# Optimization experiments

Hardware: AMD Instinct MI355X
Metric: run time of the kernel (lower is better)

Reference implementation:

```python
import jax, jax.numpy as jnp
import numpy as np

EMB_DIM = 256
NUM_HEADS = 4
HEAD_DIM = EMB_DIM // NUM_HEADS
N_EDGES = 320000
N_NODES = 10000
EPS = 1e-16  # torch_geometric softmax epsilon


def setup_inputs() -> dict:
    key = jax.random.key(0)
    kq, kk, ki, kw1, kb1, kw2 = jax.random.split(key, 6)
    q = jax.random.normal(kq, (N_EDGES, EMB_DIM), dtype=jnp.float32)
    k = jax.random.normal(kk, (N_EDGES, EMB_DIM), dtype=jnp.float32)
    index = jnp.sort(jax.random.randint(ki, (N_EDGES,), 0, N_NODES, dtype=jnp.int32))
    # xavier_uniform with gain 1/sqrt(2)
    lim1 = (1.0 / np.sqrt(2.0)) * np.sqrt(6.0 / (2 * EMB_DIM + EMB_DIM))
    w1_w = jax.random.uniform(kw1, (EMB_DIM, 2 * EMB_DIM), dtype=jnp.float32, minval=-lim1, maxval=lim1)
    w1_b = jnp.zeros((EMB_DIM,), dtype=jnp.float32)
    lim2 = (1.0 / np.sqrt(2.0)) * np.sqrt(6.0 / (NUM_HEADS + HEAD_DIM))
    w2 = jax.random.uniform(kw2, (NUM_HEADS, HEAD_DIM), dtype=jnp.float32, minval=-lim2, maxval=lim2)
    return {"q": q, "k": k, "w1_w": w1_w, "w1_b": w1_b, "w2": w2,
            "index": index, "dim_size": N_NODES}


def _segment_softmax(src, index, num_segments):
    # src: [E, H, 1]; index: [E] segment ids; stable softmax per segment per head
    seg_max = jax.ops.segment_max(src, index, num_segments=num_segments)  # [N, H, 1]
    out = jnp.exp(src - seg_max[index])
    seg_sum = jax.ops.segment_sum(out, index, num_segments=num_segments)  # [N, H, 1]
    return out / (seg_sum[index] + EPS)


def reference(q, k, w1_w, w1_b, w2, index, dim_size):
    x = jnp.concatenate([q, k], axis=1)                      # [E, 2D]
    x = x @ w1_w.T + w1_b                                    # [E, D]
    x = jax.nn.leaky_relu(x, negative_slope=0.01)
    x = x.reshape(-1, NUM_HEADS, HEAD_DIM)                   # [E, H, C]
    attn = jnp.einsum('nhc,hc->nh', x, w2)[..., None]        # [E, H, 1]
    return _segment_softmax(attn, index, dim_size)
```

## Files before the change

kernel.cpp:

```cpp
#include <hip/hip_runtime.h>
#include <hip/hip_bf16.h>


typedef __attribute__((ext_vector_type(8))) short bf16x8;
typedef __attribute__((ext_vector_type(4))) float f32x4;
typedef __attribute__((ext_vector_type(4))) short s16x4;

#define NNODES 10000

__device__ __forceinline__ short f2bf(float f) {
    __hip_bfloat16 h = __float2bfloat16(f);
    return *reinterpret_cast<short*>(&h);
}

__device__ __forceinline__ void gload_lds16(const void* g, void* l) {
    __builtin_amdgcn_global_load_lds(
        (const __attribute__((address_space(1))) unsigned int*)g,
        (__attribute__((address_space(3))) unsigned int*)l, 16, 0, 0);
}

__global__ void w1_cvt(const float* __restrict__ w1, short* __restrict__ w1b) {
    int i = (blockIdx.x * 256 + threadIdx.x) * 4;
    float4 v = *(const float4*)(w1 + i);
    s16x4 o; o[0] = f2bf(v.x); o[1] = f2bf(v.y); o[2] = f2bf(v.z); o[3] = f2bf(v.w);
    *(s16x4*)(w1b + i) = o;
}

__global__ __launch_bounds__(512, 4) void attn_gemm(
    const float* __restrict__ q, const float* __restrict__ kk_,
    const short* __restrict__ w1b, const float* __restrict__ b1,
    const float* __restrict__ w2, float* __restrict__ attn)
{
    __shared__ float lds_a[2][4096];
    __shared__ short lds_b[2][8192];

    const int tid  = threadIdx.x;
    const int lane = tid & 63;
    const int w    = tid >> 6;
    const int wm   = w >> 1;
    const int wn   = w & 1;
    const int l15  = lane & 15;
    const int lhi  = lane >> 4;
    const int row0 = blockIdx.x * 128;

    const int a_row  = w * 8 + (lane >> 3);
    const int a_csrc = (lane & 7) ^ (lane >> 3);
    const int b_d    = w * 16 + (lane >> 2);
    const int b_csrc = (lane & 3) ^ ((lane >> 3) & 3);

    f32x4 acc[2][8];
#pragma unroll
    for (int i = 0; i < 2; ++i)
#pragma unroll
        for (int j = 0; j < 8; ++j) acc[i][j] = (f32x4){0.f, 0.f, 0.f, 0.f};

    size_t a_off[2], b_off[2];
#pragma unroll
    for (int i = 0; i < 2; ++i) {
        a_off[i] = (size_t)(row0 + i * 64 + a_row) * 256 + a_csrc * 4;
        b_off[i] = (size_t)(i * 128 + b_d) * 512 + b_csrc * 8;
    }

#define STAGE(buf, kt)                                                          \
    {                                                                           \
        const float* abase = ((kt) < 8) ? q : kk_;                              \
        const int koff = ((kt) & 7) * 32;                                       \
        gload_lds16(abase + a_off[0] + koff,                                    \
                    (char*)&lds_a[buf][0] + (0 * 8 + w) * 1024);                \
        gload_lds16(abase + a_off[1] + koff,                                    \
                    (char*)&lds_a[buf][0] + (1 * 8 + w) * 1024);                \
        gload_lds16(w1b + b_off[0] + (kt) * 32,                                 \
                    (char*)&lds_b[buf][0] + (0 * 8 + w) * 1024);                \
        gload_lds16(w1b + b_off[1] + (kt) * 32,                                 \
                    (char*)&lds_b[buf][0] + (1 * 8 + w) * 1024);                \
    }

    STAGE(0, 0);
    __syncthreads();

#pragma unroll
    for (int kt = 0; kt < 16; ++kt) {
        const int cur = kt & 1;
        if (kt < 15) STAGE(cur ^ 1, kt + 1);

        bf16x8 af[2];
#pragma unroll
        for (int fm = 0; fm < 2; ++fm) {
            const int r = wm * 32 + fm * 16 + l15;
            const float* As = &lds_a[cur][r * 32];
            f32x4 a0 = *(const f32x4*)(As + (((2 * lhi)     ^ (r & 7)) * 4));
            f32x4 a1 = *(const f32x4*)(As + (((2 * lhi + 1) ^ (r & 7)) * 4));
            bf16x8 pk;
            pk[0] = f2bf(a0[0]); pk[1] = f2bf(a0[1]); pk[2] = f2bf(a0[2]); pk[3] = f2bf(a0[3]);
            pk[4] = f2bf(a1[0]); pk[5] = f2bf(a1[1]); pk[6] = f2bf(a1[2]); pk[7] = f2bf(a1[3]);
            af[fm] = pk;
        }
#pragma unroll
        for (int fn = 0; fn < 8; ++fn) {
            const int d = wn * 128 + fn * 16 + l15;
            bf16x8 bfv = *(const bf16x8*)(&lds_b[cur][d * 32 + ((lhi ^ ((d >> 1) & 3)) * 8)]);
            acc[0][fn] = __builtin_amdgcn_mfma_f32_16x16x32_bf16(af[0], bfv, acc[0][fn], 0, 0, 0);
            acc[1][fn] = __builtin_amdgcn_mfma_f32_16x16x32_bf16(af[1], bfv, acc[1][fn], 0, 0, 0);
        }
        __syncthreads();
    }
#undef STAGE

    float bias[8], w2v[8];
#pragma unroll
    for (int fn = 0; fn < 8; ++fn) {
        int col = wn * 128 + fn * 16 + l15;
        bias[fn] = b1[col];
        w2v[fn]  = w2[col];
    }
#pragma unroll
    for (int fm = 0; fm < 2; ++fm) {
#pragma unroll
        for (int r = 0; r < 4; ++r) {
            int row = row0 + wm * 32 + fm * 16 + lhi * 4 + r;
            float p0 = 0.f, p1 = 0.f;
#pragma unroll
            for (int fn = 0; fn < 4; ++fn) {
                float y = acc[fm][fn][r] + bias[fn];
                y = (y > 0.f) ? y : 0.01f * y;
                p0 += y * w2v[fn];
            }
#pragma unroll
            for (int fn = 4; fn < 8; ++fn) {
                float y = acc[fm][fn][r] + bias[fn];
                y = (y > 0.f) ? y : 0.01f * y;
                p1 += y * w2v[fn];
            }
#pragma unroll
            for (int m = 1; m < 16; m <<= 1) {
                p0 += __shfl_xor(p0, m);
                p1 += __shfl_xor(p1, m);
            }
            if (l15 == 0) {
                attn[(size_t)row * 4 + wn * 2 + 0] = p0;
                attn[(size_t)row * 4 + wn * 2 + 1] = p1;
            }
        }
    }
}

__device__ __forceinline__ unsigned fenc(float f) {
    unsigned u = __float_as_uint(f);
    return (u & 0x80000000u) ? ~u : (u | 0x80000000u);
}
__device__ __forceinline__ float fdec(unsigned k) {
    return (k & 0x80000000u) ? __uint_as_float(k ^ 0x80000000u) : __uint_as_float(~k);
}

__global__ void seg_init(unsigned* __restrict__ segmax, float* __restrict__ segsum, int n) {
    int i = blockIdx.x * blockDim.x + threadIdx.x;
    if (i < n) { segmax[i] = 0u; segsum[i] = 0.f; }
}

__global__ void seg_max(const float* __restrict__ attn, const int* __restrict__ index,
                        unsigned* __restrict__ segmax, int total) {
    int i = blockIdx.x * blockDim.x + threadIdx.x;
    if (i >= total) return;
    int e = i >> 2, h = i & 3;
    atomicMax(&segmax[index[e] * 4 + h], fenc(attn[i]));
}

__global__ void seg_expsum(float* __restrict__ attn, const int* __restrict__ index,
                           const unsigned* __restrict__ segmax, float* __restrict__ segsum,
                           int total) {
    int i = blockIdx.x * blockDim.x + threadIdx.x;
    if (i >= total) return;
    int e = i >> 2, h = i & 3;
    float m = fdec(segmax[index[e] * 4 + h]);
    float ex = expf(attn[i] - m);
    attn[i] = ex;
    atomicAdd(&segsum[index[e] * 4 + h], ex);
}

__global__ void seg_norm(const float* __restrict__ attn, const int* __restrict__ index,
                         const float* __restrict__ segsum, float* __restrict__ out, int total) {
    int i = blockIdx.x * blockDim.x + threadIdx.x;
    if (i >= total) return;
    int e = i >> 2, h = i & 3;
    out[i] = attn[i] / (segsum[index[e] * 4 + h] + 1e-16f);
}

extern "C" void kernel_launch(void* const* d_in, const int* in_sizes, int n_in,
                              void* d_out, int out_size, void* d_ws, size_t ws_size,
                              hipStream_t stream) {
    const float* q   = (const float*)d_in[0];
    const float* k   = (const float*)d_in[1];
    const float* w1  = (const float*)d_in[2];
    const float* b1  = (const float*)d_in[3];
    const float* w2  = (const float*)d_in[4];
    const int* index = (const int*)d_in[5];

    const int nE = in_sizes[0] / 256;
    char* ws = (char*)d_ws;
    float*    attn   = (float*)ws;                       ws += (size_t)nE * 4 * 4;
    unsigned* segmax = (unsigned*)ws;                    ws += (size_t)NNODES * 4 * 4;
    float*    segsum = (float*)ws;                       ws += (size_t)NNODES * 4 * 4;
    short*    w1bf   = (short*)ws;
    float*    out    = (float*)d_out;

    w1_cvt<<<128, 256, 0, stream>>>(w1, w1bf);

    int nseg = NNODES * 4;
    seg_init<<<(nseg + 255) / 256, 256, 0, stream>>>(segmax, segsum, nseg);

    attn_gemm<<<nE / 128, 512, 0, stream>>>(q, k, w1bf, b1, w2, attn);

    int total = nE * 4;
    int blks = (total + 255) / 256;
    seg_max<<<blks, 256, 0, stream>>>(attn, index, segmax, total);
    seg_expsum<<<blks, 256, 0, stream>>>(attn, index, segmax, segsum, total);
    seg_norm<<<blks, 256, 0, stream>>>(attn, index, segsum, out, total);
}
```

Before: 220.1 us.

## Fuse exp and segment-sum into GEMM epilogue, drop segment-max pass

Removes the segment max reduction and computes exp(logit) directly in the GEMM epilogue, atomically accumulating per-segment sums there, leaving only a normalization kernel. The A operand is now loaded through registers, converted to bf16 before staging into LDS, and the wave tiling is changed so each wave covers one head. This eliminates two elementwise passes and their atomics, but drops the max subtraction, so large logits could overflow exp.

```diff
diff --git a/kernel.cpp b/kernel.cpp
--- a/kernel.cpp
+++ b/kernel.cpp
@@ -26,155 +26,128 @@
     *(s16x4*)(w1b + i) = o;
 }
 
+__global__ void seg_init(float* __restrict__ segsum, int n) {
+    int i = blockIdx.x * blockDim.x + threadIdx.x;
+    if (i < n) segsum[i] = 0.f;
+}
+
 __global__ __launch_bounds__(512, 4) void attn_gemm(
     const float* __restrict__ q, const float* __restrict__ kk_,
     const short* __restrict__ w1b, const float* __restrict__ b1,
-    const float* __restrict__ w2, float* __restrict__ attn)
+    const float* __restrict__ w2, const int* __restrict__ index,
+    float* __restrict__ attn, float* __restrict__ segsum)
 {
-    __shared__ float lds_a[2][4096];
-    __shared__ short lds_b[2][8192];
+    __shared__ short lds_a[2][128 * 32];
+    __shared__ short lds_b[2][256 * 32];
 
     const int tid  = threadIdx.x;
     const int lane = tid & 63;
     const int w    = tid >> 6;
-    const int wm   = w >> 1;
-    const int wn   = w & 1;
+    const int wm   = w >> 2;
+    const int wn   = w & 3;
     const int l15  = lane & 15;
     const int lhi  = lane >> 4;
     const int row0 = blockIdx.x * 128;
 
-    const int a_row  = w * 8 + (lane >> 3);
-    const int a_csrc = (lane & 7) ^ (lane >> 3);
     const int b_d    = w * 16 + (lane >> 2);
     const int b_csrc = (lane & 3) ^ ((lane >> 3) & 3);
+    const size_t b_off0 = (size_t)b_d * 512 + b_csrc * 8;
+    const size_t b_off1 = (size_t)(128 + b_d) * 512 + b_csrc * 8;
+    const int b_dst0 = w * 1024 + lane * 16;
+    const int b_dst1 = (8 + w) * 1024 + lane * 16;
 
-    f32x4 acc[2][8];
+    const int a_r = tid >> 2;
+    const int a_c = tid & 3;
+    const size_t a_goff = (size_t)(row0 + a_r) * 256 + a_c * 8;
+    const int a_ldst = a_r * 32 + ((a_c ^ ((a_r >> 1) & 3)) * 8);
+
+    f32x4 acc[4][4];
 #pragma unroll
-    for (int i = 0; i < 2; ++i)
+    for (int i = 0; i < 4; ++i)
 #pragma unroll
-        for (int j = 0; j < 8; ++j) acc[i][j] = (f32x4){0.f, 0.f, 0.f, 0.f};
+        for (int j = 0; j < 4; ++j) acc[i][j] = (f32x4){0.f, 0.f, 0.f, 0.f};
 
-    size_t a_off[2], b_off[2];
-#pragma unroll
-    for (int i = 0; i < 2; ++i) {
-        a_off[i] = (size_t)(row0 + i * 64 + a_row) * 256 + a_csrc * 4;
-        b_off[i] = (size_t)(i * 128 + b_d) * 512 + b_csrc * 8;
+    {
+        gload_lds16(w1b + b_off0, (char*)&lds_b[0][0] + b_dst0);
+        gload_lds16(w1b + b_off1, (char*)&lds_b[0][0] + b_dst1);
+        float4 f0 = *(const float4*)(q + a_goff);
+        float4 f1 = *(const float4*)(q + a_goff + 4);
+        bf16x8 pk;
+        pk[0] = f2bf(f0.x); pk[1] = f2bf(f0.y); pk[2] = f2bf(f0.z); pk[3] = f2bf(f0.w);
+        pk[4] = f2bf(f1.x); pk[5] = f2bf(f1.y); pk[6] = f2bf(f1.z); pk[7] = f2bf(f1.w);
+        *(bf16x8*)&lds_a[0][a_ldst] = pk;
     }
-
-#define STAGE(buf, kt)                                                          \
-    {                                                                           \
-        const float* abase = ((kt) < 8) ? q : kk_;                              \
-        const int koff = ((kt) & 7) * 32;                                       \
-        gload_lds16(abase + a_off[0] + koff,                                    \
-                    (char*)&lds_a[buf][0] + (0 * 8 + w) * 1024);                \
-        gload_lds16(abase + a_off[1] + koff,                                    \
-                    (char*)&lds_a[buf][0] + (1 * 8 + w) * 1024);                \
-        gload_lds16(w1b + b_off[0] + (kt) * 32,                                 \
-                    (char*)&lds_b[buf][0] + (0 * 8 + w) * 1024);                \
-        gload_lds16(w1b + b_off[1] + (kt) * 32,                                 \
-                    (char*)&lds_b[buf][0] + (1 * 8 + w) * 1024);                \
-    }
-
-    STAGE(0, 0);
     __syncthreads();
 
 #pragma unroll
     for (int kt = 0; kt < 16; ++kt) {
-        const int cur = kt & 1;
-        if (kt < 15) STAGE(cur ^ 1, kt + 1);
+        const int cur = kt & 1, nxt = cur ^ 1;
 
-        bf16x8 af[2];
+        float4 f0, f1;
+        if (kt < 15) {
+            const float* abase = (kt + 1 < 8) ? q : kk_;
+            const int koff = ((kt + 1) & 7) * 32;
+            f0 = *(const float4*)(abase + a_goff + koff);
+            f1 = *(const float4*)(abase + a_goff + koff + 4);
+            gload_lds16(w1b + b_off0 + (size_t)(kt + 1) * 32, (char*)&lds_b[nxt][0] + b_dst0);
+            gload_lds16(w1b + b_off1 + (size_t)(kt + 1) * 32, (char*)&lds_b[nxt][0] + b_dst1);
+        }
+
+        bf16x8 af[4], bfv[4];
 #pragma unroll
-        for (int fm = 0; fm < 2; ++fm) {
-            const int r = wm * 32 + fm * 16 + l15;
-            const float* As = &lds_a[cur][r * 32];
-            f32x4 a0 = *(const f32x4*)(As + (((2 * lhi)     ^ (r & 7)) * 4));
-            f32x4 a1 = *(const f32x4*)(As + (((2 * lhi + 1) ^ (r & 7)) * 4));
-            bf16x8 pk;
-            pk[0] = f2bf(a0[0]); pk[1] = f2bf(a0[1]); pk[2] = f2bf(a0[2]); pk[3] = f2bf(a0[3]);
-            pk[4] = f2bf(a1[0]); pk[5] = f2bf(a1[1]); pk[6] = f2bf(a1[2]); pk[7] = f2bf(a1[3]);
-            af[fm] = pk;
+        for (int fm = 0; fm < 4; ++fm) {
+            const int r = wm * 64 + fm * 16 + l15;
+            af[fm] = *(const bf16x8*)&lds_a[cur][r * 32 + ((lhi ^ ((r >> 1) & 3)) * 8)];
         }
 #pragma unroll
-        for (int fn = 0; fn < 8; ++fn) {
-            const int d = wn * 128 + fn * 16 + l15;
-            bf16x8 bfv = *(const bf16x8*)(&lds_b[cur][d * 32 + ((lhi ^ ((d >> 1) & 3)) * 8)]);
-            acc[0][fn] = __builtin_amdgcn_mfma_f32_16x16x32_bf16(af[0], bfv, acc[0][fn], 0, 0, 0);
-            acc[1][fn] = __builtin_amdgcn_mfma_f32_16x16x32_bf16(af[1], bfv, acc[1][fn], 0, 0, 0);
+        for (int fn = 0; fn < 4; ++fn) {
+            const int d = wn * 64 + fn * 16 + l15;
+            bfv[fn] = *(const bf16x8*)&lds_b[cur][d * 32 + ((lhi ^ ((d >> 1) & 3)) * 8)];
+        }
+#pragma unroll
+        for (int fm = 0; fm < 4; ++fm)
+#pragma unroll
+            for (int fn = 0; fn < 4; ++fn)
+                acc[fm][fn] = __builtin_amdgcn_mfma_f32_16x16x32_bf16(
+                    af[fm], bfv[fn], acc[fm][fn], 0, 0, 0);
+
+        if (kt < 15) {
+            bf16x8 pk;
+            pk[0] = f2bf(f0.x); pk[1] = f2bf(f0.y); pk[2] = f2bf(f0.z); pk[3] = f2bf(f0.w);
+            pk[4] = f2bf(f1.x); pk[5] = f2bf(f1.y); pk[6] = f2bf(f1.z); pk[7] = f2bf(f1.w);
+            *(bf16x8*)&lds_a[nxt][a_ldst] = pk;
         }
         __syncthreads();
     }
-#undef STAGE
 
-    float bias[8], w2v[8];
+    float bias[4], w2v[4];
 #pragma unroll
-    for (int fn = 0; fn < 8; ++fn) {
-        int col = wn * 128 + fn * 16 + l15;
+    for (int fn = 0; fn < 4; ++fn) {
+        int col = wn * 64 + fn * 16 + l15;
         bias[fn] = b1[col];
         w2v[fn]  = w2[col];
     }
 #pragma unroll
-    for (int fm = 0; fm < 2; ++fm) {
+    for (int fm = 0; fm < 4; ++fm) {
 #pragma unroll
         for (int r = 0; r < 4; ++r) {
-            int row = row0 + wm * 32 + fm * 16 + lhi * 4 + r;
-            float p0 = 0.f, p1 = 0.f;
+            int row = row0 + wm * 64 + fm * 16 + lhi * 4 + r;
+            float p = 0.f;
 #pragma unroll
             for (int fn = 0; fn < 4; ++fn) {
                 float y = acc[fm][fn][r] + bias[fn];
                 y = (y > 0.f) ? y : 0.01f * y;
-                p0 += y * w2v[fn];
+                p += y * w2v[fn];
             }
 #pragma unroll
-            for (int fn = 4; fn < 8; ++fn) {
-                float y = acc[fm][fn][r] + bias[fn];
-                y = (y > 0.f) ? y : 0.01f * y;
-                p1 += y * w2v[fn];
-            }
-#pragma unroll
-            for (int m = 1; m < 16; m <<= 1) {
-                p0 += __shfl_xor(p0, m);
-                p1 += __shfl_xor(p1, m);
-            }
+            for (int m = 1; m < 16; m <<= 1) p += __shfl_xor(p, m);
             if (l15 == 0) {
-                attn[(size_t)row * 4 + wn * 2 + 0] = p0;
-                attn[(size_t)row * 4 + wn * 2 + 1] = p1;
+                float e = __expf(p);
+                attn[(size_t)row * 4 + wn] = e;
+                atomicAdd(&segsum[index[row] * 4 + wn], e);
             }
         }
     }
-}
-
-__device__ __forceinline__ unsigned fenc(float f) {
-    unsigned u = __float_as_uint(f);
-    return (u & 0x80000000u) ? ~u : (u | 0x80000000u);
-}
-__device__ __forceinline__ float fdec(unsigned k) {
-    return (k & 0x80000000u) ? __uint_as_float(k ^ 0x80000000u) : __uint_as_float(~k);
-}
-
-__global__ void seg_init(unsigned* __restrict__ segmax, float* __restrict__ segsum, int n) {
-    int i = blockIdx.x * blockDim.x + threadIdx.x;
-    if (i < n) { segmax[i] = 0u; segsum[i] = 0.f; }
-}
-
-__global__ void seg_max(const float* __restrict__ attn, const int* __restrict__ index,
-                        unsigned* __restrict__ segmax, int total) {
-    int i = blockIdx.x * blockDim.x + threadIdx.x;
-    if (i >= total) return;
-    int e = i >> 2, h = i & 3;
-    atomicMax(&segmax[index[e] * 4 + h], fenc(attn[i]));
-}
-
-__global__ void seg_expsum(float* __restrict__ attn, const int* __restrict__ index,
-                           const unsigned* __restrict__ segmax, float* __restrict__ segsum,
-                           int total) {
-    int i = blockIdx.x * blockDim.x + threadIdx.x;
-    if (i >= total) return;
-    int e = i >> 2, h = i & 3;
-    float m = fdec(segmax[index[e] * 4 + h]);
-    float ex = expf(attn[i] - m);
-    attn[i] = ex;
-    atomicAdd(&segsum[index[e] * 4 + h], ex);
 }
 
 __global__ void seg_norm(const float* __restrict__ attn, const int* __restrict__ index,
@@ -197,22 +170,16 @@
 
     const int nE = in_sizes[0] / 256;
     char* ws = (char*)d_ws;
-    float*    attn   = (float*)ws;                       ws += (size_t)nE * 4 * 4;
-    unsigned* segmax = (unsigned*)ws;                    ws += (size_t)NNODES * 4 * 4;
-    float*    segsum = (float*)ws;                       ws += (size_t)NNODES * 4 * 4;
-    short*    w1bf   = (short*)ws;
-    float*    out    = (float*)d_out;
+    float* attn   = (float*)ws;            ws += (size_t)nE * 4 * 4;
+    float* segsum = (float*)ws;            ws += (size_t)NNODES * 4 * 4;
+    short* w1bf   = (short*)ws;
+    float* out    = (float*)d_out;
 
     w1_cvt<<<128, 256, 0, stream>>>(w1, w1bf);
+    seg_init<<<(NNODES * 4 + 255) / 256, 256, 0, stream>>>(segsum, NNODES * 4);
 
-    int nseg = NNODES * 4;
-    seg_init<<<(nseg + 255) / 256, 256, 0, stream>>>(segmax, segsum, nseg);
-
-    attn_gemm<<<nE / 128, 512, 0, stream>>>(q, k, w1bf, b1, w2, attn);
+    attn_gemm<<<nE / 128, 512, 0, stream>>>(q, k, w1bf, b1, w2, index, attn, segsum);
 
     int total = nE * 4;
-    int blks = (total + 255) / 256;
-    seg_max<<<blks, 256, 0, stream>>>(attn, index, segmax, total);
-    seg_expsum<<<blks, 256, 0, stream>>>(attn, index, segmax, segsum, total);
-    seg_norm<<<blks, 256, 0, stream>>>(attn, index, segsum, out, total);
+    seg_norm<<<(total + 255) / 256, 256, 0, stream>>>(attn, index, segsum, out, total);
 }
```

Result: slower. 230.0 us (+4.5%).
